# Optimization experiments

Measured on AMD Instinct MI355X. Metric: run time of the kernel, lower is better.

## Reference

```python
import jax, jax.numpy as jnp
import numpy as np

TOL = 1e-3

def _mask(x):
    # forward = relu, backward = identity (straight-through)
    return x + jax.lax.stop_gradient(jax.nn.relu(x) - x)

def setup_inputs() -> dict:
    key = jax.random.key(0)
    ks = jax.random.split(key, 6)
    B, L, A, Y = 4096, 64, 64, 128
    return {
        "LT": jax.random.uniform(ks[0], (B, L), jnp.float32),
        "K": jax.random.uniform(ks[1], (L, A), jnp.float32),
        "AT": jax.random.uniform(ks[2], (A,), jnp.float32),
        "u": jax.random.uniform(ks[3], (L * A, Y), jnp.float32),
        "e": jax.random.uniform(ks[4], (A, Y), jnp.float32),
        "b": jax.random.uniform(ks[5], (Y,), jnp.float32),
        "max_step": 50,
    }

def _fixed_point(LT3, AT3, Km, max_step):
    # LT3: [B,L,1], AT3: [A,1] (broadcasts over batch), Km: [L,A]
    B = LT3.shape[0]
    A = Km.shape[1]
    L = Km.shape[0]
    AF0 = jnp.zeros((B, A, 1), LT3.dtype)
    LF0 = jnp.zeros((B, L, 1), LT3.dtype)

    def step_fn(AF, LF):
        Ldi = LT3 / (jnp.matmul(Km, AF) + 1.0)          # [B,L,1]
        Adi = AT3 / (jnp.matmul(Km.T, LF) + 1.0)        # [B,A,1]
        AF_n = AT3 / (jnp.matmul(Km.T, Ldi) + 1.0)      # [B,A,1]
        LF_n = LT3 / (jnp.matmul(Km, Adi) + 1.0)        # [B,L,1]
        return AF_n, LF_n

    def cond(state):
        step, _, _, err = state
        return jnp.logical_and(step < max_step, err >= TOL)

    def body(state):
        step, AF, LF, _ = state
        AF_n, LF_n = step_fn(AF, LF)
        err = (jnp.max(jnp.abs(AF_n - AF) / (AF + 1e-5)) +
               jnp.max(jnp.abs(LF_n - LF) / (LF + 1e-5)))
        return (step + 1, AF_n, LF_n, err)

    _, AF, LF, _ = jax.lax.while_loop(cond, body, (0, AF0, LF0, jnp.array(jnp.inf, LT3.dtype)))
    return AF, LF

def reference(LT, K, AT, u, e, b, max_step):
    Km = _mask(K)            # [L,A]
    ATm = _mask(AT)          # [A]
    B = LT.shape[0]
    LT3 = LT[:, :, None]     # [B,L,1]
    AT3 = ATm[:, None]       # [A,1]

    # fixed-point loop was under torch.no_grad(): feed stop_gradient'd values
    AF, LF = _fixed_point(jax.lax.stop_gradient(LT3),
                          jax.lax.stop_gradient(AT3),
                          jax.lax.stop_gradient(Km), max_step)

    # final differentiable refinement step
    Ldi = LT3 / (jnp.matmul(Km, AF) + 1.0)
    Adi = AT3 / (jnp.matmul(Km.T, LF) + 1.0)
    AFf = AT3 / (jnp.matmul(Km.T, Ldi) + 1.0)   # [B,A,1]
    LFf = LT3 / (jnp.matmul(Km, Adi) + 1.0)     # [B,L,1]

    AFt = jnp.swapaxes(AFf, 1, 2)               # [B,1,A]
    D = (Km * jnp.matmul(LFf, AFt)).reshape(B, -1)   # [B, L*A]
    AFsq = AFt[:, 0, :]                          # [B,A]
    y = D @ u + AFsq @ e + b[None, :]            # [B,Y]
    return y
```

## Files before the change

### kernel.cpp

```cpp
#include <hip/hip_runtime.h>
#include <hip/hip_bf16.h>

typedef __bf16 bf16x8 __attribute__((ext_vector_type(8)));
typedef __bf16 bf16x4 __attribute__((ext_vector_type(4)));
typedef float  float4v __attribute__((ext_vector_type(4)));

#define MFMA16 __builtin_amdgcn_mfma_f32_16x16x32_bf16
#define W2T_STRIDE 4160

__device__ __forceinline__ float bf2f(unsigned short u){
  union { unsigned int i; float f; } x; x.i = ((unsigned int)u) << 16; return x.f;
}
__device__ __forceinline__ unsigned short f2bf(float f){
  union { float f; unsigned int i; } x; x.f = f;
  unsigned int r = x.i + 0x7FFFu + ((x.i >> 16) & 1u);
  return (unsigned short)(r >> 16);
}
__device__ __forceinline__ float ldin(const void* p, int i, bool isbf){
  return isbf ? bf2f(((const unsigned short*)p)[i]) : ((const float*)p)[i];
}
__device__ __forceinline__ float frcp(float x){ return __builtin_amdgcn_rcpf(x); }


template<bool SPLIT>
__device__ __forceinline__ void halfstep(
    const bf16x8 (&A)[4][2], const float4v (&V)[4],
    __bf16* sH, __bf16* sL, int rb, int wb)
{
  bf16x8 bh0 = *(const bf16x8*)(sH + rb);
  bf16x8 bh1 = *(const bf16x8*)(sH + rb + 32);
  const float4v ones = {1.f, 1.f, 1.f, 1.f};
  float4v c[4];
  #pragma unroll
  for (int T = 0; T < 4; ++T) c[T] = MFMA16(A[T][0], bh0, ones, 0, 0, 0);
  #pragma unroll
  for (int T = 0; T < 4; ++T) c[T] = MFMA16(A[T][1], bh1, c[T], 0, 0, 0);
  if (SPLIT){
    bf16x8 bl0 = *(const bf16x8*)(sL + rb);
    bf16x8 bl1 = *(const bf16x8*)(sL + rb + 32);
    const float4v zero = {0.f, 0.f, 0.f, 0.f};
    float4v d[4];
    #pragma unroll
    for (int T = 0; T < 4; ++T) d[T] = MFMA16(A[T][0], bl0, zero, 0, 0, 0);
    #pragma unroll
    for (int T = 0; T < 4; ++T) d[T] = MFMA16(A[T][1], bl1, d[T], 0, 0, 0);
    #pragma unroll
    for (int T = 0; T < 4; ++T) c[T] += d[T];
  }
  #pragma unroll
  for (int T = 0; T < 4; ++T){
    bf16x4 h, lo;
    #pragma unroll
    for (int r = 0; r < 4; ++r){
      float o = V[T][r] * frcp(c[T][r]);
      __bf16 hh = (__bf16)o;
      h[r] = hh;
      if (SPLIT) lo[r] = (__bf16)(o - (float)hh);
    }
    *(bf16x4*)(sH + wb + 16 * T) = h;
    if (SPLIT) *(bf16x4*)(sL + wb + 16 * T) = lo;
  }
}

__global__ __launch_bounds__(128) void k_fused(
    const void* LT, const void* K, const void* AT, const void* u,
    const void* e, const int* msin,
    __bf16* gAF, __bf16* gLF, __bf16* W2T)
{
  __shared__ __attribute__((aligned(16))) char smem[25856];
  const int tid = threadIdx.x, bid = blockIdx.x;

  int ok = 0;
  if (tid < 64){
    float v = bf2f(((const unsigned short*)AT)[tid]);
    ok = (v >= 0.f && v <= 1.0f) ? 1 : 0;
  }
  int cnt = __syncthreads_count(ok);
  const bool isbf = (cnt >= 60);

  if (bid >= 256){
    if (bid < 384){
      float* sT = (float*)smem;
      const int ub = bid - 256;
      const int kl = tid & 63;
      for (int t2 = 0; t2 < 2; ++t2){
        const int t = ub * 2 + t2;
        const int k0 = (t >> 2) * 64, y0 = (t & 3) * 32, l = t >> 2;
        __syncthreads();
        #pragma unroll
        for (int i = 0; i < 16; ++i){
          int flat = i * 128 + tid, r = flat >> 5, c = flat & 31;
          sT[r * 33 + c] = ldin(u, (k0 + r) * 128 + y0 + c, isbf);
        }
        __syncthreads();
        float kmv = ldin(K, l * 64 + kl, isbf); kmv = fmaxf(kmv, 0.f);
        #pragma unroll
        for (int i = 0; i < 16; ++i){
          int yl = 2 * i + (tid >> 6);
          W2T[(y0 + yl) * W2T_STRIDE + k0 + kl] = (__bf16)(kmv * sT[kl * 33 + yl]);
        }
      }
    } else {
      float* sE = (float*)smem;
      const int y0 = (bid - 384) * 64;
      const int kl = tid & 63;
      #pragma unroll
      for (int i = 0; i < 32; ++i){
        int flat = i * 128 + tid, a = flat >> 6, c = flat & 63;
        sE[a * 65 + c] = ldin(e, a * 128 + y0 + c, isbf);
      }
      __syncthreads();
      #pragma unroll
      for (int i = 0; i < 32; ++i){
        int yl = 2 * i + (tid >> 6);
        W2T[(y0 + yl) * W2T_STRIDE + 4096 + kl] = (__bf16)sE[kl * 65 + yl];
      }
    }
    return;
  }

  float* sKf = (float*)smem;
  #pragma unroll
  for (int i = 0; i < 32; ++i){
    int idx = i * 128 + tid, l = idx >> 6, a = idx & 63;
    float v = ldin(K, idx, isbf);
    sKf[l * 65 + a] = fmaxf(v, 0.f);
  }
  __syncthreads();

  const int w = tid >> 6, lane = tid & 63;
  const int lr = lane & 15, q = lane >> 4;
  const int row0 = bid * 16;
  __bf16* sH = (__bf16*)(smem + 16640 + w * 4608);
  __bf16* sL = sH + 2304 / 2;

  const bf16x4 z4 = {(__bf16)0.f, (__bf16)0.f, (__bf16)0.f, (__bf16)0.f};
  for (int i = lane; i < 288; i += 64){
    *(bf16x4*)(sH + 4 * i) = z4;
    *(bf16x4*)(sL + 4 * i) = z4;
  }

  bf16x8 a1[4][2], a2[4][2];
  #pragma unroll
  for (int T = 0; T < 4; ++T)
    #pragma unroll
    for (int ks = 0; ks < 2; ++ks){
      bf16x8 f1, f2;
      #pragma unroll
      for (int j = 0; j < 8; ++j){
        float vKm = sKf[(16 * T + lr) * 65 + ks * 32 + q * 8 + j];
        float vKT = sKf[(ks * 32 + q * 8 + j) * 65 + 16 * T + lr];
        f1[j] = (__bf16)(w ? vKT : vKm);
        f2[j] = (__bf16)(w ? vKm : vKT);
      }
      a1[T][ks] = f1; a2[T][ks] = f2;
    }

  float4v ltv[4], atv[4];
  if (isbf){
    const unsigned short* lt = (const unsigned short*)LT + (row0 + lr) * 64;
    const unsigned short* at = (const unsigned short*)AT;
    #pragma unroll
    for (int T = 0; T < 4; ++T)
      #pragma unroll
      for (int r = 0; r < 4; ++r){
        int d = 16 * T + q * 4 + r;
        ltv[T][r] = bf2f(lt[d]);
        atv[T][r] = fmaxf(bf2f(at[d]), 0.f);
      }
  } else {
    const float* lt = (const float*)LT + (row0 + lr) * 64;
    const float* at = (const float*)AT;
    #pragma unroll
    for (int T = 0; T < 4; ++T){
      ltv[T] = *(const float4v*)(lt + 16 * T + q * 4);
      float4v a = *(const float4v*)(at + 16 * T + q * 4);
      #pragma unroll
      for (int r = 0; r < 4; ++r) atv[T][r] = fmaxf(a[r], 0.f);
    }
  }
  float4v V1[4], V2[4];
  #pragma unroll
  for (int T = 0; T < 4; ++T){
    V1[T] = w ? atv[T] : ltv[T];
    V2[T] = w ? ltv[T] : atv[T];
  }

  int mi = msin[0];
  if (mi <= 0 || mi > 1000000){
    float mf = ((const float*)msin)[0];
    mi = (mf > 0.f && mf < 1.0e6f) ? (int)mf : 50;
  }

  const int rb = lr * 72 + q * 8;
  const int wb = lr * 72 + q * 4;

  const int nPlain = mi > 6 ? mi - 6 : 0;
  const int nSplit = mi - nPlain;
  for (int s = 0; s < nPlain; ++s){
    halfstep<false>(a1, V1, sH, sL, rb, wb);
    halfstep<false>(a2, V2, sH, sL, rb, wb);
  }
  for (int s = 0; s < nSplit; ++s){
    halfstep<true>(a1, V1, sH, sL, rb, wb);
    halfstep<true>(a2, V2, sH, sL, rb, wb);
  }
  halfstep<true>(a1, V1, sH, sL, rb, wb);
  halfstep<true>(a2, V2, sH, sL, rb, wb);

  __bf16* gX = (w ? gLF : gAF) + row0 * 64;
  const int lrow = lane >> 2, seg = lane & 3;
  bf16x8 v0 = *(const bf16x8*)(sH + lrow * 72 + seg * 16);
  bf16x8 v1 = *(const bf16x8*)(sH + lrow * 72 + seg * 16 + 8);
  *(bf16x8*)(gX + lrow * 64 + seg * 16) = v0;
  *(bf16x8*)(gX + lrow * 64 + seg * 16 + 8) = v1;
}

__global__ __launch_bounds__(256) void k_epi(
    const __bf16* gAF, const __bf16* gLF, const __bf16* W2T,
    const void* bvec, void* out)
{
  __shared__ __attribute__((aligned(16))) __bf16 sAF[64 * 72], sLF[64 * 72];
  const int tid = threadIdx.x, wv = tid >> 6, lane = tid & 63;
  const int lr = lane & 15, q = lane >> 4;

  int ok = 0;
  if (tid < 64){
    float v = bf2f(((const unsigned short*)bvec)[tid]);
    ok = (v >= 0.f && v <= 1.0f) ? 1 : 0;
  }
  int cnt = __syncthreads_count(ok);
  const bool isbf = (cnt >= 60);

  const int rg = blockIdx.x >> 1, yh = blockIdx.x & 1;
  const int rows0 = rg * 64;
  {
    int lrow = tid >> 2, seg = tid & 3;
    *(bf16x8*)(sAF + lrow * 72 + seg * 16) =
        *(const bf16x8*)(gAF + (rows0 + lrow) * 64 + seg * 16);
    *(bf16x8*)(sAF + lrow * 72 + seg * 16 + 8) =
        *(const bf16x8*)(gAF + (rows0 + lrow) * 64 + seg * 16 + 8);
    *(bf16x8*)(sLF + lrow * 72 + seg * 16) =
        *(const bf16x8*)(gLF + (rows0 + lrow) * 64 + seg * 16);
    *(bf16x8*)(sLF + lrow * 72 + seg * 16 + 8) =
        *(const bf16x8*)(gLF + (rows0 + lrow) * 64 + seg * 16 + 8);
  }
  __syncthreads();

  const int r0w = (wv & 1) * 32;
  const int y0 = yh * 64 + (wv >> 1) * 32;

  const float bv0 = ldin(bvec, y0 + lr, isbf);
  const float bv1 = ldin(bvec, y0 + 16 + lr, isbf);
  float4v acc[2][2];
  acc[0][0] = float4v{bv0, bv0, bv0, bv0};
  acc[0][1] = float4v{bv1, bv1, bv1, bv1};
  acc[1][0] = acc[0][0];
  acc[1][1] = acc[0][1];

  bf16x8 afr[2][2];
  float aff[2][2][8];
  #pragma unroll
  for (int at = 0; at < 2; ++at){
    const int rloc = r0w + at * 16 + lr;
    afr[at][0] = *(const bf16x8*)(sAF + rloc * 72 + q * 8);
    afr[at][1] = *(const bf16x8*)(sAF + rloc * 72 + 32 + q * 8);
    #pragma unroll
    for (int j = 0; j < 8; ++j){
      aff[at][0][j] = (float)afr[at][0][j];
      aff[at][1][j] = (float)afr[at][1][j];
    }
  }

  const __bf16* w0 = W2T + (y0 + lr) * W2T_STRIDE + q * 8;
  const __bf16* w1 = w0 + 16 * W2T_STRIDE;

  #pragma unroll 2
  for (int l = 0; l < 64; ++l){
    const float lf0 = (float)sLF[(r0w + lr) * 72 + l];
    const float lf1 = (float)sLF[(r0w + 16 + lr) * 72 + l];
    bf16x8 aD[2][2];
    #pragma unroll
    for (int j = 0; j < 8; ++j){
      aD[0][0][j] = (__bf16)(lf0 * aff[0][0][j]);
      aD[0][1][j] = (__bf16)(lf0 * aff[0][1][j]);
      aD[1][0][j] = (__bf16)(lf1 * aff[1][0][j]);
      aD[1][1][j] = (__bf16)(lf1 * aff[1][1][j]);
    }
    const int kb = l * 64;
    bf16x8 b00 = *(const bf16x8*)(w0 + kb);
    bf16x8 b01 = *(const bf16x8*)(w0 + kb + 32);
    bf16x8 b10 = *(const bf16x8*)(w1 + kb);
    bf16x8 b11 = *(const bf16x8*)(w1 + kb + 32);
    acc[0][0] = MFMA16(aD[0][0], b00, acc[0][0], 0, 0, 0);
    acc[0][0] = MFMA16(aD[0][1], b01, acc[0][0], 0, 0, 0);
    acc[0][1] = MFMA16(aD[0][0], b10, acc[0][1], 0, 0, 0);
    acc[0][1] = MFMA16(aD[0][1], b11, acc[0][1], 0, 0, 0);
    acc[1][0] = MFMA16(aD[1][0], b00, acc[1][0], 0, 0, 0);
    acc[1][0] = MFMA16(aD[1][1], b01, acc[1][0], 0, 0, 0);
    acc[1][1] = MFMA16(aD[1][0], b10, acc[1][1], 0, 0, 0);
    acc[1][1] = MFMA16(aD[1][1], b11, acc[1][1], 0, 0, 0);
  }
  {
    bf16x8 b00 = *(const bf16x8*)(w0 + 4096);
    bf16x8 b01 = *(const bf16x8*)(w0 + 4096 + 32);
    bf16x8 b10 = *(const bf16x8*)(w1 + 4096);
    bf16x8 b11 = *(const bf16x8*)(w1 + 4096 + 32);
    #pragma unroll
    for (int at = 0; at < 2; ++at){
      acc[at][0] = MFMA16(afr[at][0], b00, acc[at][0], 0, 0, 0);
      acc[at][0] = MFMA16(afr[at][1], b01, acc[at][0], 0, 0, 0);
      acc[at][1] = MFMA16(afr[at][0], b10, acc[at][1], 0, 0, 0);
      acc[at][1] = MFMA16(afr[at][1], b11, acc[at][1], 0, 0, 0);
    }
  }

  if (isbf){
    unsigned short* o = (unsigned short*)out;
    #pragma unroll
    for (int at = 0; at < 2; ++at)
      #pragma unroll
      for (int r = 0; r < 4; ++r){
        int orow = rows0 + r0w + at * 16 + q * 4 + r;
        o[orow * 128 + y0 + lr]      = f2bf(acc[at][0][r]);
        o[orow * 128 + y0 + 16 + lr] = f2bf(acc[at][1][r]);
      }
  } else {
    float* o = (float*)out;
    #pragma unroll
    for (int at = 0; at < 2; ++at)
      #pragma unroll
      for (int r = 0; r < 4; ++r){
        int orow = rows0 + r0w + at * 16 + q * 4 + r;
        o[orow * 128 + y0 + lr]      = acc[at][0][r];
        o[orow * 128 + y0 + 16 + lr] = acc[at][1][r];
      }
  }
}

extern "C" void kernel_launch(void* const* d_in, const int* in_sizes, int n_in,
                              void* d_out, int out_size, void* d_ws, size_t ws_size,
                              hipStream_t stream){
  char* ws = (char*)d_ws;
  __bf16* gAF = (__bf16*)(ws);
  __bf16* gLF = (__bf16*)(ws + 524288);
  __bf16* W2T = (__bf16*)(ws + 1048576);

  k_fused<<<dim3(386), dim3(128), 0, stream>>>(
      d_in[0], d_in[1], d_in[2], d_in[3], d_in[4], (const int*)d_in[6],
      gAF, gLF, W2T);
  k_epi<<<dim3(128), dim3(256), 0, stream>>>(
      gAF, gLF, W2T, d_in[5], d_out);
}
```

Before: 140.0 us.

## Switch to fp16 register-resident fixed point with per-wave early exit, halve epilogue tiles

Moves the fixed-point iteration and the epilogue from bf16 to fp16 MFMA. The iterate now stays in registers via a permuted K fragment layout, which removes the LDS round trips and the hi/lo split correction passes. Each wave adds a per-step convergence check with a ballot so it can stop before max_step. The epilogue uses half-size row tiles and twice the blocks for more parallelism. Risks: fp16 overflow or precision loss, and the per-wave convergence test differs from the reference's global max criterion.

After: 117.0 us. -16.4%, faster.

```diff
diff --git a/kernel.cpp b/kernel.cpp
--- a/kernel.cpp
+++ b/kernel.cpp
@@ -1,13 +1,21 @@
 #include <hip/hip_runtime.h>
 #include <hip/hip_bf16.h>
 
-typedef __bf16 bf16x8 __attribute__((ext_vector_type(8)));
-typedef __bf16 bf16x4 __attribute__((ext_vector_type(4)));
+typedef _Float16 half8 __attribute__((ext_vector_type(8)));
+typedef _Float16 h2    __attribute__((ext_vector_type(2)));
 typedef float  float4v __attribute__((ext_vector_type(4)));
 
-#define MFMA16 __builtin_amdgcn_mfma_f32_16x16x32_bf16
-#define W2T_STRIDE 4160
-
+#define MFMAH __builtin_amdgcn_mfma_f32_16x16x32_f16
+#define W2S 4160
+
+union U8 { half8 v; h2 p[4]; int i[4]; };
+
+__device__ __forceinline__ h2 pkrtz(float a, float b){
+  auto r = __builtin_amdgcn_cvt_pkrtz(a, b);
+  h2 o;
+  __builtin_memcpy(&o, &r, sizeof(o));
+  return o;
+}
 __device__ __forceinline__ float bf2f(unsigned short u){
   union { unsigned int i; float f; } x; x.i = ((unsigned int)u) << 16; return x.f;
 }
@@ -22,52 +30,66 @@
 __device__ __forceinline__ float frcp(float x){ return __builtin_amdgcn_rcpf(x); }
 
 
-template<bool SPLIT>
-__device__ __forceinline__ void halfstep(
-    const bf16x8 (&A)[4][2], const float4v (&V)[4],
-    __bf16* sH, __bf16* sL, int rb, int wb)
+__device__ __forceinline__ void hstep_plain(const half8 (&A)[4][2], const float4v (&V)[4],
+                                            half8& B0, half8& B1)
 {
-  bf16x8 bh0 = *(const bf16x8*)(sH + rb);
-  bf16x8 bh1 = *(const bf16x8*)(sH + rb + 32);
-  const float4v ones = {1.f, 1.f, 1.f, 1.f};
+  const float4v ones = {1.f,1.f,1.f,1.f};
   float4v c[4];
   #pragma unroll
-  for (int T = 0; T < 4; ++T) c[T] = MFMA16(A[T][0], bh0, ones, 0, 0, 0);
-  #pragma unroll
-  for (int T = 0; T < 4; ++T) c[T] = MFMA16(A[T][1], bh1, c[T], 0, 0, 0);
-  if (SPLIT){
-    bf16x8 bl0 = *(const bf16x8*)(sL + rb);
-    bf16x8 bl1 = *(const bf16x8*)(sL + rb + 32);
-    const float4v zero = {0.f, 0.f, 0.f, 0.f};
-    float4v d[4];
-    #pragma unroll
-    for (int T = 0; T < 4; ++T) d[T] = MFMA16(A[T][0], bl0, zero, 0, 0, 0);
-    #pragma unroll
-    for (int T = 0; T < 4; ++T) d[T] = MFMA16(A[T][1], bl1, d[T], 0, 0, 0);
-    #pragma unroll
-    for (int T = 0; T < 4; ++T) c[T] += d[T];
-  }
+  for (int T = 0; T < 4; ++T) c[T] = MFMAH(A[T][0], B0, ones, 0, 0, 0);
+  #pragma unroll
+  for (int T = 0; T < 4; ++T) c[T] = MFMAH(A[T][1], B1, c[T], 0, 0, 0);
+  U8 n0, n1;
   #pragma unroll
   for (int T = 0; T < 4; ++T){
-    bf16x4 h, lo;
+    float o0 = V[T][0] * frcp(c[T][0]);
+    float o1 = V[T][1] * frcp(c[T][1]);
+    float o2 = V[T][2] * frcp(c[T][2]);
+    float o3 = V[T][3] * frcp(c[T][3]);
+    h2 pa = pkrtz(o0, o1);
+    h2 pb = pkrtz(o2, o3);
+    if (T < 2){ n0.p[2*T] = pa; n0.p[2*T+1] = pb; }
+    else      { n1.p[2*(T-2)] = pa; n1.p[2*(T-2)+1] = pb; }
+  }
+  B0 = n0.v; B1 = n1.v;
+}
+
+__device__ __forceinline__ float hstep_err(const half8 (&A)[4][2], const float4v (&V)[4],
+                                           half8& B0, half8& B1, float4v (&old)[4])
+{
+  const float4v ones = {1.f,1.f,1.f,1.f};
+  float4v c[4];
+  #pragma unroll
+  for (int T = 0; T < 4; ++T) c[T] = MFMAH(A[T][0], B0, ones, 0, 0, 0);
+  #pragma unroll
+  for (int T = 0; T < 4; ++T) c[T] = MFMAH(A[T][1], B1, c[T], 0, 0, 0);
+  U8 n0, n1;
+  float worst = -1.f;
+  #pragma unroll
+  for (int T = 0; T < 4; ++T){
+    float4v o;
     #pragma unroll
     for (int r = 0; r < 4; ++r){
-      float o = V[T][r] * frcp(c[T][r]);
-      __bf16 hh = (__bf16)o;
-      h[r] = hh;
-      if (SPLIT) lo[r] = (__bf16)(o - (float)hh);
-    }
-    *(bf16x4*)(sH + wb + 16 * T) = h;
-    if (SPLIT) *(bf16x4*)(sL + wb + 16 * T) = lo;
-  }
-}
-
-__global__ __launch_bounds__(128) void k_fused(
+      o[r] = V[T][r] * frcp(c[T][r]);
+      float thr = old[T][r] * 6e-4f + 6e-9f;
+      worst = fmaxf(worst, fabsf(o[r] - old[T][r]) - thr);
+    }
+    old[T] = o;
+    h2 pa = pkrtz(o[0], o[1]);
+    h2 pb = pkrtz(o[2], o[3]);
+    if (T < 2){ n0.p[2*T] = pa; n0.p[2*T+1] = pb; }
+    else      { n1.p[2*(T-2)] = pa; n1.p[2*(T-2)+1] = pb; }
+  }
+  B0 = n0.v; B1 = n1.v;
+  return worst;
+}
+
+__global__ __launch_bounds__(128, 1) void k_fused(
     const void* LT, const void* K, const void* AT, const void* u,
     const void* e, const int* msin,
-    __bf16* gAF, __bf16* gLF, __bf16* W2T)
+    _Float16* gAF, _Float16* gLF, _Float16* W2T)
 {
-  __shared__ __attribute__((aligned(16))) char smem[25856];
+  __shared__ __attribute__((aligned(16))) float sKf[64 * 65];
   const int tid = threadIdx.x, bid = blockIdx.x;
 
   int ok = 0;
@@ -80,7 +102,7 @@
 
   if (bid >= 256){
     if (bid < 384){
-      float* sT = (float*)smem;
+      float* sT = sKf;
       const int ub = bid - 256;
       const int kl = tid & 63;
       for (int t2 = 0; t2 < 2; ++t2){
@@ -97,11 +119,11 @@
         #pragma unroll
         for (int i = 0; i < 16; ++i){
           int yl = 2 * i + (tid >> 6);
-          W2T[(y0 + yl) * W2T_STRIDE + k0 + kl] = (__bf16)(kmv * sT[kl * 33 + yl]);
+          W2T[(y0 + yl) * W2S + k0 + kl] = (_Float16)(kmv * sT[kl * 33 + yl]);
         }
       }
     } else {
-      float* sE = (float*)smem;
+      float* sE = sKf;
       const int y0 = (bid - 384) * 64;
       const int kl = tid & 63;
       #pragma unroll
@@ -113,45 +135,37 @@
       #pragma unroll
       for (int i = 0; i < 32; ++i){
         int yl = 2 * i + (tid >> 6);
-        W2T[(y0 + yl) * W2T_STRIDE + 4096 + kl] = (__bf16)sE[kl * 65 + yl];
+        W2T[(y0 + yl) * W2S + 4096 + kl] = (_Float16)sE[kl * 65 + yl];
       }
     }
     return;
   }
 
-  float* sKf = (float*)smem;
   #pragma unroll
   for (int i = 0; i < 32; ++i){
     int idx = i * 128 + tid, l = idx >> 6, a = idx & 63;
-    float v = ldin(K, idx, isbf);
-    sKf[l * 65 + a] = fmaxf(v, 0.f);
+    sKf[l * 65 + a] = fmaxf(ldin(K, idx, isbf), 0.f);
   }
   __syncthreads();
 
   const int w = tid >> 6, lane = tid & 63;
   const int lr = lane & 15, q = lane >> 4;
   const int row0 = bid * 16;
-  __bf16* sH = (__bf16*)(smem + 16640 + w * 4608);
-  __bf16* sL = sH + 2304 / 2;
-
-  const bf16x4 z4 = {(__bf16)0.f, (__bf16)0.f, (__bf16)0.f, (__bf16)0.f};
-  for (int i = lane; i < 288; i += 64){
-    *(bf16x4*)(sH + 4 * i) = z4;
-    *(bf16x4*)(sL + 4 * i) = z4;
-  }
-
-  bf16x8 a1[4][2], a2[4][2];
+
+  half8 a1[4][2], a2[4][2];
   #pragma unroll
   for (int T = 0; T < 4; ++T)
     #pragma unroll
     for (int ks = 0; ks < 2; ++ks){
-      bf16x8 f1, f2;
+      half8 f1, f2;
       #pragma unroll
       for (int j = 0; j < 8; ++j){
-        float vKm = sKf[(16 * T + lr) * 65 + ks * 32 + q * 8 + j];
-        float vKT = sKf[(ks * 32 + q * 8 + j) * 65 + 16 * T + lr];
-        f1[j] = (__bf16)(w ? vKT : vKm);
-        f2[j] = (__bf16)(w ? vKm : vKT);
+        int kcol = ks * 32 + ((j >> 2) * 16) + q * 4 + (j & 3);
+        int row  = 16 * T + lr;
+        float vKm = sKf[row * 65 + kcol];
+        float vKT = sKf[kcol * 65 + row];
+        f1[j] = (_Float16)(w ? vKT : vKm);
+        f2[j] = (_Float16)(w ? vKm : vKT);
       }
       a1[T][ks] = f1; a2[T][ks] = f2;
     }
@@ -187,40 +201,40 @@
   }
 
   int mi = msin[0];
-  if (mi <= 0 || mi > 1000000){
+  if (mi < 0 || mi > 1000000){
     float mf = ((const float*)msin)[0];
-    mi = (mf > 0.f && mf < 1.0e6f) ? (int)mf : 50;
-  }
-
-  const int rb = lr * 72 + q * 8;
-  const int wb = lr * 72 + q * 4;
-
-  const int nPlain = mi > 6 ? mi - 6 : 0;
-  const int nSplit = mi - nPlain;
-  for (int s = 0; s < nPlain; ++s){
-    halfstep<false>(a1, V1, sH, sL, rb, wb);
-    halfstep<false>(a2, V2, sH, sL, rb, wb);
-  }
-  for (int s = 0; s < nSplit; ++s){
-    halfstep<true>(a1, V1, sH, sL, rb, wb);
-    halfstep<true>(a2, V2, sH, sL, rb, wb);
-  }
-  halfstep<true>(a1, V1, sH, sL, rb, wb);
-  halfstep<true>(a2, V2, sH, sL, rb, wb);
-
-  __bf16* gX = (w ? gLF : gAF) + row0 * 64;
-  const int lrow = lane >> 2, seg = lane & 3;
-  bf16x8 v0 = *(const bf16x8*)(sH + lrow * 72 + seg * 16);
-  bf16x8 v1 = *(const bf16x8*)(sH + lrow * 72 + seg * 16 + 8);
-  *(bf16x8*)(gX + lrow * 64 + seg * 16) = v0;
-  *(bf16x8*)(gX + lrow * 64 + seg * 16 + 8) = v1;
+    mi = (mf >= 0.f && mf < 1.0e6f) ? (int)mf : 50;
+  }
+
+  half8 B0 = {}, B1 = {};
+  float4v old[4] = {};
+
+  int conv = 0;
+  for (int s = 0; s < mi && !conv; ++s){
+    hstep_plain(a1, V1, B0, B1);
+    float worst = hstep_err(a2, V2, B0, B1, old);
+    conv = (__ballot(worst > 0.f) == 0ULL) ? 1 : 0;
+  }
+  hstep_plain(a1, V1, B0, B1);
+  hstep_plain(a2, V2, B0, B1);
+
+  _Float16* gX = (w ? gLF : gAF) + (row0 + lr) * 64;
+  int* g32 = (int*)gX;
+  U8 ub0, ub1; ub0.v = B0; ub1.v = B1;
+  #pragma unroll
+  for (int T = 0; T < 4; ++T){
+    int base = 8 * T + 2 * q;
+    const U8& s = (T < 2) ? ub0 : ub1;
+    g32[base]     = s.i[2 * (T & 1)];
+    g32[base + 1] = s.i[2 * (T & 1) + 1];
+  }
 }
 
 __global__ __launch_bounds__(256) void k_epi(
-    const __bf16* gAF, const __bf16* gLF, const __bf16* W2T,
+    const _Float16* gAF, const _Float16* gLF, const _Float16* W2T,
     const void* bvec, void* out)
 {
-  __shared__ __attribute__((aligned(16))) __bf16 sAF[64 * 72], sLF[64 * 72];
+  __shared__ __attribute__((aligned(16))) _Float16 sAF[32 * 72], sLF[32 * 72];
   const int tid = threadIdx.x, wv = tid >> 6, lane = tid & 63;
   const int lr = lane & 15, q = lane >> 4;
 
@@ -232,109 +246,79 @@
   int cnt = __syncthreads_count(ok);
   const bool isbf = (cnt >= 60);
 
-  const int rg = blockIdx.x >> 1, yh = blockIdx.x & 1;
-  const int rows0 = rg * 64;
+  const int rows0 = (blockIdx.x >> 1) * 32, yh = blockIdx.x & 1;
   {
-    int lrow = tid >> 2, seg = tid & 3;
-    *(bf16x8*)(sAF + lrow * 72 + seg * 16) =
-        *(const bf16x8*)(gAF + (rows0 + lrow) * 64 + seg * 16);
-    *(bf16x8*)(sAF + lrow * 72 + seg * 16 + 8) =
-        *(const bf16x8*)(gAF + (rows0 + lrow) * 64 + seg * 16 + 8);
-    *(bf16x8*)(sLF + lrow * 72 + seg * 16) =
-        *(const bf16x8*)(gLF + (rows0 + lrow) * 64 + seg * 16);
-    *(bf16x8*)(sLF + lrow * 72 + seg * 16 + 8) =
-        *(const bf16x8*)(gLF + (rows0 + lrow) * 64 + seg * 16 + 8);
+    int lrow = tid >> 3, seg = tid & 7;
+    *(half8*)(sAF + lrow * 72 + seg * 8) =
+        *(const half8*)(gAF + (rows0 + lrow) * 64 + seg * 8);
+    *(half8*)(sLF + lrow * 72 + seg * 8) =
+        *(const half8*)(gLF + (rows0 + lrow) * 64 + seg * 8);
   }
   __syncthreads();
 
-  const int r0w = (wv & 1) * 32;
+  const int r0 = (wv & 1) * 16;
   const int y0 = yh * 64 + (wv >> 1) * 32;
+  const int rloc = r0 + lr;
 
   const float bv0 = ldin(bvec, y0 + lr, isbf);
   const float bv1 = ldin(bvec, y0 + 16 + lr, isbf);
-  float4v acc[2][2];
-  acc[0][0] = float4v{bv0, bv0, bv0, bv0};
-  acc[0][1] = float4v{bv1, bv1, bv1, bv1};
-  acc[1][0] = acc[0][0];
-  acc[1][1] = acc[0][1];
-
-  bf16x8 afr[2][2];
-  float aff[2][2][8];
-  #pragma unroll
-  for (int at = 0; at < 2; ++at){
-    const int rloc = r0w + at * 16 + lr;
-    afr[at][0] = *(const bf16x8*)(sAF + rloc * 72 + q * 8);
-    afr[at][1] = *(const bf16x8*)(sAF + rloc * 72 + 32 + q * 8);
-    #pragma unroll
-    for (int j = 0; j < 8; ++j){
-      aff[at][0][j] = (float)afr[at][0][j];
-      aff[at][1][j] = (float)afr[at][1][j];
-    }
-  }
-
-  const __bf16* w0 = W2T + (y0 + lr) * W2T_STRIDE + q * 8;
-  const __bf16* w1 = w0 + 16 * W2T_STRIDE;
-
-  #pragma unroll 2
+  float4v acc0 = {bv0, bv0, bv0, bv0};
+  float4v acc1 = {bv1, bv1, bv1, bv1};
+
+  U8 uaf0, uaf1;
+  uaf0.v = *(const half8*)(sAF + rloc * 72 + q * 8);
+  uaf1.v = *(const half8*)(sAF + rloc * 72 + 32 + q * 8);
+
+  const _Float16* w0 = W2T + (y0 + lr) * W2S + q * 8;
+  const _Float16* w1 = w0 + 16 * W2S;
+
+  #pragma unroll 4
   for (int l = 0; l < 64; ++l){
-    const float lf0 = (float)sLF[(r0w + lr) * 72 + l];
-    const float lf1 = (float)sLF[(r0w + 16 + lr) * 72 + l];
-    bf16x8 aD[2][2];
-    #pragma unroll
-    for (int j = 0; j < 8; ++j){
-      aD[0][0][j] = (__bf16)(lf0 * aff[0][0][j]);
-      aD[0][1][j] = (__bf16)(lf0 * aff[0][1][j]);
-      aD[1][0][j] = (__bf16)(lf1 * aff[1][0][j]);
-      aD[1][1][j] = (__bf16)(lf1 * aff[1][1][j]);
+    _Float16 lfv = sLF[rloc * 72 + l];
+    h2 lf2 = {lfv, lfv};
+    U8 d0, d1;
+    #pragma unroll
+    for (int i = 0; i < 4; ++i){
+      d0.p[i] = lf2 * uaf0.p[i];
+      d1.p[i] = lf2 * uaf1.p[i];
     }
     const int kb = l * 64;
-    bf16x8 b00 = *(const bf16x8*)(w0 + kb);
-    bf16x8 b01 = *(const bf16x8*)(w0 + kb + 32);
-    bf16x8 b10 = *(const bf16x8*)(w1 + kb);
-    bf16x8 b11 = *(const bf16x8*)(w1 + kb + 32);
-    acc[0][0] = MFMA16(aD[0][0], b00, acc[0][0], 0, 0, 0);
-    acc[0][0] = MFMA16(aD[0][1], b01, acc[0][0], 0, 0, 0);
-    acc[0][1] = MFMA16(aD[0][0], b10, acc[0][1], 0, 0, 0);
-    acc[0][1] = MFMA16(aD[0][1], b11, acc[0][1], 0, 0, 0);
-    acc[1][0] = MFMA16(aD[1][0], b00, acc[1][0], 0, 0, 0);
-    acc[1][0] = MFMA16(aD[1][1], b01, acc[1][0], 0, 0, 0);
-    acc[1][1] = MFMA16(aD[1][0], b10, acc[1][1], 0, 0, 0);
-    acc[1][1] = MFMA16(aD[1][1], b11, acc[1][1], 0, 0, 0);
+    half8 b00 = *(const half8*)(w0 + kb);
+    half8 b01 = *(const half8*)(w0 + kb + 32);
+    half8 b10 = *(const half8*)(w1 + kb);
+    half8 b11 = *(const half8*)(w1 + kb + 32);
+    acc0 = MFMAH(d0.v, b00, acc0, 0, 0, 0);
+    acc0 = MFMAH(d1.v, b01, acc0, 0, 0, 0);
+    acc1 = MFMAH(d0.v, b10, acc1, 0, 0, 0);
+    acc1 = MFMAH(d1.v, b11, acc1, 0, 0, 0);
   }
   {
-    bf16x8 b00 = *(const bf16x8*)(w0 + 4096);
-    bf16x8 b01 = *(const bf16x8*)(w0 + 4096 + 32);
-    bf16x8 b10 = *(const bf16x8*)(w1 + 4096);
-    bf16x8 b11 = *(const bf16x8*)(w1 + 4096 + 32);
-    #pragma unroll
-    for (int at = 0; at < 2; ++at){
-      acc[at][0] = MFMA16(afr[at][0], b00, acc[at][0], 0, 0, 0);
-      acc[at][0] = MFMA16(afr[at][1], b01, acc[at][0], 0, 0, 0);
-      acc[at][1] = MFMA16(afr[at][0], b10, acc[at][1], 0, 0, 0);
-      acc[at][1] = MFMA16(afr[at][1], b11, acc[at][1], 0, 0, 0);
-    }
+    half8 b00 = *(const half8*)(w0 + 4096);
+    half8 b01 = *(const half8*)(w0 + 4096 + 32);
+    half8 b10 = *(const half8*)(w1 + 4096);
+    half8 b11 = *(const half8*)(w1 + 4096 + 32);
+    acc0 = MFMAH(uaf0.v, b00, acc0, 0, 0, 0);
+    acc0 = MFMAH(uaf1.v, b01, acc0, 0, 0, 0);
+    acc1 = MFMAH(uaf0.v, b10, acc1, 0, 0, 0);
+    acc1 = MFMAH(uaf1.v, b11, acc1, 0, 0, 0);
   }
 
   if (isbf){
     unsigned short* o = (unsigned short*)out;
     #pragma unroll
-    for (int at = 0; at < 2; ++at)
-      #pragma unroll
-      for (int r = 0; r < 4; ++r){
-        int orow = rows0 + r0w + at * 16 + q * 4 + r;
-        o[orow * 128 + y0 + lr]      = f2bf(acc[at][0][r]);
-        o[orow * 128 + y0 + 16 + lr] = f2bf(acc[at][1][r]);
-      }
+    for (int r = 0; r < 4; ++r){
+      int orow = rows0 + r0 + q * 4 + r;
+      o[orow * 128 + y0 + lr]      = f2bf(acc0[r]);
+      o[orow * 128 + y0 + 16 + lr] = f2bf(acc1[r]);
+    }
   } else {
     float* o = (float*)out;
     #pragma unroll
-    for (int at = 0; at < 2; ++at)
-      #pragma unroll
-      for (int r = 0; r < 4; ++r){
-        int orow = rows0 + r0w + at * 16 + q * 4 + r;
-        o[orow * 128 + y0 + lr]      = acc[at][0][r];
-        o[orow * 128 + y0 + 16 + lr] = acc[at][1][r];
-      }
+    for (int r = 0; r < 4; ++r){
+      int orow = rows0 + r0 + q * 4 + r;
+      o[orow * 128 + y0 + lr]      = acc0[r];
+      o[orow * 128 + y0 + 16 + lr] = acc1[r];
+    }
   }
 }
 
@@ -342,13 +326,13 @@
                               void* d_out, int out_size, void* d_ws, size_t ws_size,
                               hipStream_t stream){
   char* ws = (char*)d_ws;
-  __bf16* gAF = (__bf16*)(ws);
-  __bf16* gLF = (__bf16*)(ws + 524288);
-  __bf16* W2T = (__bf16*)(ws + 1048576);
+  _Float16* gAF = (_Float16*)(ws);
+  _Float16* gLF = (_Float16*)(ws + 524288);
+  _Float16* W2T = (_Float16*)(ws + 1048576);
 
   k_fused<<<dim3(386), dim3(128), 0, stream>>>(
       d_in[0], d_in[1], d_in[2], d_in[3], d_in[4], (const int*)d_in[6],
       gAF, gLF, W2T);
-  k_epi<<<dim3(128), dim3(256), 0, stream>>>(
+  k_epi<<<dim3(256), dim3(256), 0, stream>>>(
       gAF, gLF, W2T, d_in[5], d_out);
 }
```
